# Kernel tuning notes

Hardware: AMD Instinct MI355X
Metric: run time of the kernel (lower is better)

Reference implementation:

```python
import jax, jax.numpy as jnp
import numpy as np

NUM_ENTITY = 500000
NUM_RELATION = 6000
NUM_WORD = 200000
D = 100          # entity_dim == word_dim
L = 3            # num_layer
B, E, F, Q = 16, 2000, 8000, 20
PAGERANK_LAMBDA = 0.8
FACT_SCALE = 3.0
VERY_NEG = -1e11
VERY_SMALL = 1e-10


def setup_inputs() -> dict:
    key = jax.random.key(0)
    ks = jax.random.split(key, 24)
    s = 0.05
    return {
        'local_entity': jax.random.randint(ks[0], (B, E), 0, NUM_ENTITY),
        'kb_fact_rel': jax.random.randint(ks[1], (B, F), 0, NUM_RELATION),
        'kb_head': jax.random.randint(ks[2], (B, F), 0, E),
        'kb_tail': jax.random.randint(ks[3], (B, F), 0, E),
        'query_text': jax.random.randint(ks[4], (B, Q), 0, NUM_WORD),
        'q2e_adj_mat': jax.random.uniform(ks[5], (B, E, 1)),
        'entity_table': jax.random.normal(ks[6], (NUM_ENTITY + 1, D)) * s,
        'rel_table': jax.random.normal(ks[7], (NUM_RELATION + 1, D)) * s,
        'word_table': jax.random.normal(ks[8], (NUM_WORD + 1, D)) * s,
        'rel_lin_w': jax.random.normal(ks[9], (D, D)) * s,
        'rel_lin_b': jnp.zeros((D,)),
        'lstm_wih': jax.random.normal(ks[10], (4 * D, D)) * s,
        'lstm_whh': jax.random.normal(ks[11], (4 * D, D)) * s,
        'lstm_bih': jnp.zeros((4 * D,)),
        'lstm_bhh': jnp.zeros((4 * D,)),
        'q2e_w': jax.random.normal(ks[12], (L, D, D)) * s,
        'q2e_b': jnp.zeros((L, D)),
        'e2q_w': jax.random.normal(ks[13], (L, D, 3 * D)) * s,
        'e2q_b': jnp.zeros((L, D)),
        'e2e_w': jax.random.normal(ks[14], (L, D, 3 * D)) * s,
        'e2e_b': jnp.zeros((L, D)),
        'head_w': jax.random.normal(ks[15], (L, D, D)) * s,
        'head_b': jnp.zeros((L, D)),
        'tail_w': jax.random.normal(ks[16], (L, D, D)) * s,
        'tail_b': jnp.zeros((L, D)),
        'self_w': jax.random.normal(ks[17], (L, D, D)) * s,
        'self_b': jnp.zeros((L, D)),
        'score_w': jax.random.normal(ks[18], (1, D)) * s,
        'score_b': jnp.zeros((1,)),
    }


def _lstm(x, wih, whh, bih, bhh):
    # x: (B, Q, D); torch LSTM gate order i,f,g,o
    b = x.shape[0]
    h0 = jnp.zeros((b, D), x.dtype)

    def step(carry, xt):
        h, c = carry
        g = xt @ wih.T + h @ whh.T + bih + bhh
        i, f, gg, o = jnp.split(g, 4, axis=-1)
        c = jax.nn.sigmoid(f) * c + jax.nn.sigmoid(i) * jnp.tanh(gg)
        h = jax.nn.sigmoid(o) * jnp.tanh(c)
        return (h, c), h

    (h, _), hs = jax.lax.scan(step, (h0, h0), x.transpose(1, 0, 2))
    return hs.transpose(1, 0, 2), h


def _gather(x, idx):
    # sparse_bmm(entity2fact, x): out[b,f] = x[b, head[b,f]]
    return jnp.take_along_axis(x, idx[:, :, None], axis=1)


def _scatter(x, idx, num):
    # sparse_bmm(fact2entity, x): segment-sum facts onto tail entities
    b, f, d = x.shape
    flat = (idx + jnp.arange(b)[:, None] * num).reshape(-1)
    return jax.ops.segment_sum(x.reshape(b * f, d), flat, num_segments=b * num).reshape(b, num, d)


def reference(local_entity, kb_fact_rel, kb_head, kb_tail, query_text, q2e_adj_mat,
              entity_table, rel_table, word_table, rel_lin_w, rel_lin_b,
              lstm_wih, lstm_whh, lstm_bih, lstm_bhh,
              q2e_w, q2e_b, e2q_w, e2q_b, e2e_w, e2e_b,
              head_w, head_b, tail_w, tail_b, self_w, self_b, score_w, score_b):
    div = float(np.sqrt(D))
    q_mask = (query_text != NUM_WORD).astype(jnp.float32)
    e_mask = (local_entity != NUM_ENTITY).astype(jnp.float32)

    # query LSTM encoding
    q_emb = word_table[query_text]                                   # (B,Q,D)
    q_hidden, q_last = _lstm(q_emb, lstm_wih, lstm_whh, lstm_bih, lstm_bhh)
    query_node_emb = q_last[:, None, :]                              # (B,1,D)

    # fact embeddings from relations
    fact_emb = rel_table[kb_fact_rel] @ rel_lin_w.T + rel_lin_b      # (B,F,D)

    # fact-to-query attention weights (softmax over query words)
    sim = jnp.einsum('bqd,bfd->bqf', q_hidden, fact_emb) / div
    sim = jax.nn.softmax(sim + (1.0 - q_mask)[:, :, None] * VERY_NEG, axis=1)
    att = jnp.einsum('bqf,bqd->bfd', sim, q_hidden)                  # (B,F,D)
    Wf = jnp.sum(att * fact_emb, axis=2) / div                       # (B,F)
    W_tilde = jnp.exp(Wf - Wf.max(axis=1, keepdims=True))
    e2f_softmax = jnp.clip(_scatter(W_tilde[:, :, None], kb_head, E)[:, :, 0], VERY_SMALL, None)

    local_entity_emb = entity_table[local_entity]                    # (B,E,D)
    pagerank_f = q2e_adj_mat[:, :, 0]                                # (B,E)

    for i in range(L):
        q2e_emb = jnp.broadcast_to(query_node_emb @ q2e_w[i].T + q2e_b[i], (B, E, D))
        # entity -> fact (gather heads)
        e2f = jax.nn.relu(fact_emb @ self_w[i].T + self_b[i] +
                          _gather(local_entity_emb @ head_w[i].T + head_b[i], kb_head))
        e2f = e2f * (W_tilde[:, :, None] * _gather((pagerank_f / e2f_softmax)[:, :, None], kb_head))
        # fact -> entity (scatter to tails)
        f2e = jax.nn.relu(local_entity_emb @ self_w[i].T + self_b[i] +
                          FACT_SCALE * _scatter(e2f @ tail_w[i].T + tail_b[i], kb_tail, E))
        # pagerank propagation
        pr = _scatter(_gather(pagerank_f[:, :, None], kb_head), kb_tail, E)[:, :, 0]
        pagerank_f = PAGERANK_LAMBDA * pr + (1.0 - PAGERANK_LAMBDA) * pagerank_f
        # k=3 concat -> e2q / e2e updates
        nxt = jnp.concatenate([local_entity_emb, q2e_emb, f2e], axis=2)   # (B,E,3D)
        query_node_emb = jnp.einsum('be,bed->bd', pagerank_f, nxt @ e2q_w[i].T + e2q_b[i])[:, None, :]
        local_entity_emb = jax.nn.relu(nxt @ e2e_w[i].T + e2e_b[i])

    score = (local_entity_emb @ score_w.T + score_b)[:, :, 0]
    return score + (1.0 - e_mask) * VERY_NEG
```

## Files before the change

### kernel.cpp

```cpp
#include <hip/hip_runtime.h>
#include <math.h>

namespace {

typedef unsigned short u16;
typedef short bf16x8 __attribute__((ext_vector_type(8)));
typedef float f32x4 __attribute__((ext_vector_type(4)));

constexpr int B = 16, E = 2000, F = 8000, Q = 20, D = 100, NLAYER = 3;
constexpr int NUM_ENTITY_C = 500000;
constexpr int NREL1 = 6001;
constexpr int SK = 128;
constexpr int WFSZ = 28 * 64 * 8;
constexpr float PAGERANK_LAMBDA = 0.8f;
constexpr float FACT_SCALE = 3.0f;
constexpr float VERY_NEG = -100000000000.0f;
constexpr float VERY_SMALL = 1e-10f;

__device__ __forceinline__ float sigf(float x) { return 1.0f / (1.0f + __expf(-x)); }

__device__ __forceinline__ short f2bf(float f) {
    union { float f; unsigned int u; } c; c.f = f;
    unsigned int u = c.u + 0x7FFF + ((c.u >> 16) & 1);
    return (short)(u >> 16);
}
__device__ __forceinline__ float bf2f(u16 s) {
    union { unsigned int u; float f; } c; c.u = ((unsigned int)s) << 16;
    return c.f;
}

__global__ void wprep_kernel(const float* __restrict__ rel_lin_w,
                             const float* __restrict__ self_w, const float* __restrict__ head_w,
                             const float* __restrict__ tail_w, const float* __restrict__ e2e_w,
                             u16* __restrict__ WF)
{
    int m = blockIdx.y;
    int ns = blockIdx.x;
    int n = ns >> 2, s = ns & 3;
    int lane = threadIdx.x;
    const float* W; int ldW = D, kofs = 0; float scale = 1.f;
    if (m == 0) { W = rel_lin_w; }
    else {
        int L = (m - 1) / 5, t = (m - 1) % 5;
        if (t == 0)      { W = self_w + (size_t)L * D * D; }
        else if (t == 1) { W = head_w + (size_t)L * D * D; }
        else if (t == 2) { W = tail_w + (size_t)L * D * D; scale = FACT_SCALE; }
        else if (t == 3) { W = e2e_w + (size_t)L * D * 3 * D; ldW = 3 * D; }
        else             { W = e2e_w + (size_t)L * D * 3 * D; ldW = 3 * D; kofs = 2 * D; }
    }
    int col = n * 16 + (lane & 15);
    int kb = s * 32 + (lane >> 4) * 8;
    bf16x8 f;
#pragma unroll
    for (int j = 0; j < 8; ++j) {
        int k = kb + j;
        float v = (col < D && k < D) ? scale * W[(size_t)col * ldW + kofs + k] : 0.f;
        f[j] = f2bf(v);
    }
    *reinterpret_cast<bf16x8*>(WF + ((size_t)m * 28 + ns) * 64 * 8 + lane * 8) = f;
}

template<int A1S, int A2S, int EPI, bool OUTBF>
__global__ __launch_bounds__(256, 2) void mm2(
    const void* __restrict__ A1p, const int* __restrict__ idx1, int lda1,
    const void* __restrict__ A2p, const int* __restrict__ idx2,
    const u16* __restrict__ WF1, const u16* __restrict__ WF2,
    const float* __restrict__ b1, const float* __restrict__ b2,
    const float* __restrict__ vq,
    const float* __restrict__ wtv, const float* __restrict__ prv,
    const float* __restrict__ e2fsmv,
    const int* __restrict__ row_start, const int* __restrict__ factlist,
    const float* __restrict__ prOld, const int* __restrict__ headAbs,
    float* __restrict__ prNew,
    void* __restrict__ outp, int nrows)
{
    const int lane = threadIdx.x & 63;
    const int lrow = lane & 15, lkg = lane >> 4;
    const int wv = blockIdx.x * (blockDim.x >> 6) + (threadIdx.x >> 6);
    const int nwv = gridDim.x * (blockDim.x >> 6);
    const int nch = (nrows + 15) >> 4;

    bf16x8 w1[7][4];
#pragma unroll
    for (int n = 0; n < 7; ++n)
#pragma unroll
        for (int s = 0; s < 4; ++s)
            w1[n][s] = *reinterpret_cast<const bf16x8*>(WF1 + ((size_t)(n * 4 + s) * 64 + lane) * 8);

    for (int chunk = wv; chunk < nch; chunk += nwv) {
        const int row = chunk * 16 + lrow;
        const int ar = row < nrows ? row : nrows - 1;

        bf16x8 af1[4];
        if (A1S == 0) {
            const u16* src = (const u16*)A1p + (size_t)ar * SK;
#pragma unroll
            for (int s = 0; s < 4; ++s)
                af1[s] = *reinterpret_cast<const bf16x8*>(src + s * 32 + lkg * 8);
        } else if (A1S == 1) {
            const u16* src = (const u16*)A1p + (size_t)idx1[ar] * SK;
#pragma unroll
            for (int s = 0; s < 4; ++s)
                af1[s] = *reinterpret_cast<const bf16x8*>(src + s * 32 + lkg * 8);
        } else {
            const float* arow = (const float*)A1p + (size_t)ar * lda1;
#pragma unroll
            for (int s = 0; s < 4; ++s) {
                const int k0 = s * 32 + lkg * 8;
                float tv[8];
                if (k0 + 8 <= D) {
                    float4 v0 = *reinterpret_cast<const float4*>(arow + k0);
                    float4 v1 = *reinterpret_cast<const float4*>(arow + k0 + 4);
                    tv[0]=v0.x; tv[1]=v0.y; tv[2]=v0.z; tv[3]=v0.w;
                    tv[4]=v1.x; tv[5]=v1.y; tv[6]=v1.z; tv[7]=v1.w;
                } else {
#pragma unroll
                    for (int j = 0; j < 8; ++j) tv[j] = (k0 + j < D) ? arow[k0 + j] : 0.f;
                }
                bf16x8 f;
#pragma unroll
                for (int j = 0; j < 8; ++j) f[j] = f2bf(tv[j]);
                af1[s] = f;
            }
        }

        bf16x8 af2[4];
        if (A2S == 1) {
            const u16* src = (const u16*)A2p + (size_t)idx2[ar] * SK;
#pragma unroll
            for (int s = 0; s < 4; ++s)
                af2[s] = *reinterpret_cast<const bf16x8*>(src + s * 32 + lkg * 8);
        } else if (A2S == 3) {
            const u16* src = (const u16*)A2p + (size_t)ar * SK;
#pragma unroll
            for (int s = 0; s < 4; ++s)
                af2[s] = *reinterpret_cast<const bf16x8*>(src + s * 32 + lkg * 8);
        } else if (A2S == 2) {
            float a2f[4][8];
#pragma unroll
            for (int s = 0; s < 4; ++s)
#pragma unroll
                for (int j = 0; j < 8; ++j) a2f[s][j] = 0.f;
            const int s0 = row_start[ar], s1 = row_start[ar + 1];
            for (int i = s0; i < s1; ++i) {
                const u16* fr = (const u16*)A2p + (size_t)factlist[i] * SK + lkg * 8;
#pragma unroll
                for (int s = 0; s < 4; ++s) {
                    bf16x8 v = *reinterpret_cast<const bf16x8*>(fr + s * 32);
#pragma unroll
                    for (int j = 0; j < 8; ++j) a2f[s][j] += bf2f((u16)v[j]);
                }
            }
#pragma unroll
            for (int s = 0; s < 4; ++s) {
                bf16x8 f;
#pragma unroll
                for (int j = 0; j < 8; ++j) f[j] = f2bf(a2f[s][j]);
                af2[s] = f;
            }
            if (lkg == 0 && row < nrows) {
                float a = 0.f;
                for (int i = s0; i < s1; ++i) a += prOld[headAbs[factlist[i]]];
                prNew[row] = PAGERANK_LAMBDA * a + (1.0f - PAGERANK_LAMBDA) * prOld[row];
            }
        }

        f32x4 acc[7];
#pragma unroll
        for (int n = 0; n < 7; ++n) acc[n] = (f32x4){0.f, 0.f, 0.f, 0.f};
#pragma unroll
        for (int s = 0; s < 4; ++s) {
#pragma unroll
            for (int n = 0; n < 7; ++n)
                acc[n] = __builtin_amdgcn_mfma_f32_16x16x32_bf16(af1[s], w1[n][s], acc[n], 0, 0, 0);
            if (A2S != 0) {
#pragma unroll
                for (int n = 0; n < 7; ++n) {
                    bf16x8 w2 = *reinterpret_cast<const bf16x8*>(
                        WF2 + ((size_t)(n * 4 + s) * 64 + lane) * 8);
                    acc[n] = __builtin_amdgcn_mfma_f32_16x16x32_bf16(af2[s], w2, acc[n], 0, 0, 0);
                }
            }
        }

        const int rb = chunk * 16 + lkg * 4;
#pragma unroll
        for (int r = 0; r < 4; ++r) {
            const int orow = rb + r;
            if (orow >= nrows) continue;
            float rsv = 1.f, cntf = 0.f; int vb = 0;
            if (EPI == 1) {
                int h = idx2[orow];
                rsv = wtv[orow] * prv[h] / fmaxf(e2fsmv[h], VERY_SMALL);
            }
            if (EPI == 2) cntf = (float)(row_start[orow + 1] - row_start[orow]);
            if (EPI == 3) vb = orow / E;
#pragma unroll
            for (int n = 0; n < 7; ++n) {
                const int col = n * 16 + lrow;
                if (col >= D) continue;
                float v = acc[n][r];
                if (b1) v += b1[col];
                if (EPI == 1) v += b2[col];
                if (EPI == 2) v += FACT_SCALE * cntf * b2[col];
                if (EPI == 3) v += vq[vb * D + col];
                if (EPI != 0) v = fmaxf(v, 0.f);
                if (EPI == 1) v *= rsv;
                if (OUTBF) ((u16*)outp)[(size_t)orow * SK + col] = (u16)f2bf(v);
                else       ((float*)outp)[(size_t)orow * D + col] = v;
            }
        }
    }
}

__global__ __launch_bounds__(512) void gatesx_kernel(
    const int* __restrict__ qtext, const float* __restrict__ wtab,
    const float* __restrict__ wih, const float* __restrict__ bih,
    const float* __restrict__ bhh, float* __restrict__ gx)
{
    int row = blockIdx.x;
    int t = threadIdx.x;
    __shared__ __align__(16) float xs[D];
    if (t < D) xs[t] = wtab[(size_t)qtext[row] * D + t];
    __syncthreads();
    if (t < 4 * D) {
        const float4* w4 = reinterpret_cast<const float4*>(wih + (size_t)t * D);
        const float4* x4 = reinterpret_cast<const float4*>(xs);
        float a0 = 0.f, a1 = 0.f, a2 = 0.f, a3 = 0.f;
#pragma unroll
        for (int k = 0; k < 25; ++k) {
            float4 wv = w4[k]; float4 xv = x4[k];
            a0 = fmaf(wv.x, xv.x, a0); a1 = fmaf(wv.y, xv.y, a1);
            a2 = fmaf(wv.z, xv.z, a2); a3 = fmaf(wv.w, xv.w, a3);
        }
        gx[(size_t)row * (4 * D) + t] = a0 + a1 + a2 + a3 + bih[t] + bhh[t];
    }
}

__global__ __launch_bounds__(512) void lstmrec_kernel(
    const float* __restrict__ gx, const float* __restrict__ whh,
    float* __restrict__ q_hidden, float* __restrict__ qne)
{
    int b = blockIdx.x, t = threadIdx.x;
    __shared__ __align__(16) float h[D];
    __shared__ float cst[D];
    __shared__ float g[4 * D];
    float4 w[25];
    if (t < 4 * D) {
        const float4* wr = reinterpret_cast<const float4*>(whh + (size_t)t * D);
#pragma unroll
        for (int k = 0; k < 25; ++k) w[k] = wr[k];
    }
    if (t < D) { h[t] = 0.f; cst[t] = 0.f; }
    __syncthreads();
    for (int step = 0; step < Q; ++step) {
        if (t < 4 * D) {
            const float4* h4 = reinterpret_cast<const float4*>(h);
            float a0 = 0.f, a1 = 0.f, a2 = 0.f, a3 = 0.f;
#pragma unroll
            for (int k = 0; k < 25; ++k) {
                float4 hv = h4[k];
                a0 = fmaf(w[k].x, hv.x, a0); a1 = fmaf(w[k].y, hv.y, a1);
                a2 = fmaf(w[k].z, hv.z, a2); a3 = fmaf(w[k].w, hv.w, a3);
            }
            g[t] = a0 + a1 + a2 + a3 + gx[((size_t)b * Q + step) * (4 * D) + t];
        }
        __syncthreads();
        if (t < D) {
            float gi = g[t], gf = g[t + D], gg = g[t + 2 * D], go = g[t + 3 * D];
            float cn = sigf(gf) * cst[t] + sigf(gi) * tanhf(gg);
            float hn = sigf(go) * tanhf(cn);
            cst[t] = cn; h[t] = hn;
            q_hidden[((size_t)b * Q + step) * D + t] = hn;
            if (step == Q - 1) qne[b * D + t] = hn;
        }
        __syncthreads();
    }
}

__global__ __launch_bounds__(256) void wf_kernel(const float* __restrict__ qh,
                                                 const u16* __restrict__ REL,
                                                 const int* __restrict__ frel,
                                                 float* __restrict__ Wf)
{
    const int b = blockIdx.y;
    const int f0 = blockIdx.x * 128;
    __shared__ float qs[Q * D];
    __shared__ float fs[128 * 106];
    const int tid = threadIdx.x;
    for (int i = tid; i < Q * D; i += 256) qs[i] = qh[(size_t)b * Q * D + i];
    for (int i = tid; i < 128 * 16; i += 256) {
        int r = i >> 4, c = i & 15;
        if (c < 13 && f0 + r < F) {
            const u16* src = REL + (size_t)frel[b * F + f0 + r] * SK + c * 8;
            bf16x8 raw = *reinterpret_cast<const bf16x8*>(src);
#pragma unroll
            for (int j = 0; j < 8; ++j) fs[r * 106 + c * 8 + j] = bf2f((u16)raw[j]);
        }
    }
    __syncthreads();
    const int f = tid >> 1, half = tid & 1;
    const float* frow = &fs[f * 106 + half * 50];
    float s[Q];
#pragma unroll
    for (int q = 0; q < Q; ++q) {
        const float* qrow = &qs[q * D + half * 50];
        float accv = 0.f;
#pragma unroll 5
        for (int k = 0; k < 50; ++k) accv = fmaf(qrow[k], frow[k], accv);
        accv += __shfl_xor(accv, 1);
        s[q] = accv * 0.1f;
    }
    float mx = s[0];
#pragma unroll
    for (int q = 1; q < Q; ++q) mx = fmaxf(mx, s[q]);
    float sum = 0.f, wf = 0.f;
#pragma unroll
    for (int q = 0; q < Q; ++q) {
        float p = __expf(s[q] - mx);
        sum += p; wf = fmaf(p, s[q], wf);
    }
    wf /= sum;
    if (half == 0 && f0 + f < F) Wf[(size_t)b * F + f0 + f] = wf;
}

__global__ void idxabs_kernel(const int* __restrict__ kb_head, const int* __restrict__ kb_tail,
                              int* __restrict__ headAbs, int* __restrict__ tailAbs,
                              int* __restrict__ counts)
{
    int r = blockIdx.x * 256 + threadIdx.x;
    if (r < B * F) {
        int b = r / F;
        headAbs[r] = b * E + kb_head[r];
        int t = b * E + kb_tail[r];
        tailAbs[r] = t;
        atomicAdd(&counts[t], 1);
    }
}

__global__ __launch_bounds__(1024) void scan_kernel(const int* __restrict__ counts,
                                                    int* __restrict__ row_start,
                                                    int* __restrict__ cursor)
{
    __shared__ int part[1024];
    int t = threadIdx.x;
    int base = t * 32;
    int local[32];
    int s = 0;
#pragma unroll
    for (int i = 0; i < 32; ++i) {
        int idx = base + i;
        int v = (idx < B * E) ? counts[idx] : 0;
        local[i] = s; s += v;
    }
    part[t] = s;
    __syncthreads();
    for (int off = 1; off < 1024; off <<= 1) {
        int v = (t >= off) ? part[t - off] : 0;
        __syncthreads();
        if (t >= off) part[t] += v;
        __syncthreads();
    }
    int prev = (t > 0) ? part[t - 1] : 0;
#pragma unroll
    for (int i = 0; i < 32; ++i) {
        int idx = base + i;
        if (idx < B * E) { int rs = prev + local[i]; row_start[idx] = rs; cursor[idx] = rs; }
    }
    if (t == 1023) row_start[B * E] = part[1023];
}

__global__ void fill_kernel(const int* __restrict__ tailAbs, int* __restrict__ cursor,
                            int* __restrict__ factlist)
{
    int r = blockIdx.x * 256 + threadIdx.x;
    if (r < B * F) {
        int p = atomicAdd(&cursor[tailAbs[r]], 1);
        factlist[p] = r;
    }
}

__global__ void rowmax_kernel(const float* __restrict__ Wf, float* __restrict__ Wmax)
{
    int b = blockIdx.x, tid = threadIdx.x;
    float m = -3.4e38f;
    for (int i = tid; i < F; i += 256) m = fmaxf(m, Wf[(size_t)b * F + i]);
#pragma unroll
    for (int o = 32; o > 0; o >>= 1) m = fmaxf(m, __shfl_down(m, o));
    __shared__ float sm[4];
    if ((tid & 63) == 0) sm[tid >> 6] = m;
    __syncthreads();
    if (tid == 0) Wmax[b] = fmaxf(fmaxf(sm[0], sm[1]), fmaxf(sm[2], sm[3]));
}

__global__ void wtilde_kernel(float* __restrict__ wt, const float* __restrict__ Wmax,
                              const int* __restrict__ headAbs, float* __restrict__ e2fsm)
{
    int r = blockIdx.x * 256 + threadIdx.x;
    if (r < B * F) {
        int b = r / F;
        float v = __expf(wt[r] - Wmax[b]);
        wt[r] = v;
        atomicAdd(&e2fsm[headAbs[r]], v);
    }
}

__global__ void entgather_kernel(const int* __restrict__ local_entity,
                                 const float* __restrict__ etab, u16* __restrict__ emb,
                                 const float* __restrict__ q2e_adj, float* __restrict__ pr)
{
    int i = blockIdx.x * 256 + threadIdx.x;
    if (i < B * E) pr[i] = q2e_adj[i];
    if (i < B * E * 25) {
        int row = i / 25, p = i - row * 25;
        float4 v = reinterpret_cast<const float4*>(etab + (size_t)local_entity[row] * D)[p];
        short4 o;
        o.x = f2bf(v.x); o.y = f2bf(v.y); o.z = f2bf(v.z); o.w = f2bf(v.w);
        *reinterpret_cast<short4*>(emb + (size_t)row * SK + p * 4) = o;
    }
}

__global__ void qvec_kernel(const float* __restrict__ qne, const float* __restrict__ q2ew,
                            const float* __restrict__ q2eb, const float* __restrict__ e2ew,
                            float* __restrict__ q2e_vec, float* __restrict__ vq)
{
    int b = blockIdx.x, t = threadIdx.x;
    __shared__ float qv[D];
    __shared__ float qn[D];
    if (t < D) qn[t] = qne[b * D + t];
    __syncthreads();
    if (t < D) {
        const float* wr = q2ew + (size_t)t * D;
        float acc = q2eb[t];
        for (int k = 0; k < D; ++k) acc = fmaf(qn[k], wr[k], acc);
        qv[t] = acc; q2e_vec[b * D + t] = acc;
    }
    __syncthreads();
    if (t < D) {
        const float* wr = e2ew + (size_t)t * 300 + 100;
        float acc = 0.f;
        for (int k = 0; k < D; ++k) acc = fmaf(qv[k], wr[k], acc);
        vq[b * D + t] = acc;
    }
}

__global__ __launch_bounds__(256) void zsum_kernel(const float* __restrict__ pr,
                                                   const u16* __restrict__ emb,
                                                   const u16* __restrict__ f2e,
                                                   float* __restrict__ zpart)
{
    const int b = blockIdx.x, ch = blockIdx.y;
    const int t = threadIdx.x;
    const int g = t >> 4, tg = t & 15;
    const int ebase = ch * (E / 16);
    const int eend = ebase + (E / 16);
    float accA[8], accB[8];
#pragma unroll
    for (int j = 0; j < 8; ++j) { accA[j] = 0.f; accB[j] = 0.f; }
    float accp = 0.f;
    for (int e = ebase + g; e < eend; e += 16) {
        const float p = pr[b * E + e];
        const size_t ro = ((size_t)b * E + e) * SK + tg * 8;
        bf16x8 va = *reinterpret_cast<const bf16x8*>(emb + ro);
        bf16x8 vb = *reinterpret_cast<const bf16x8*>(f2e + ro);
#pragma unroll
        for (int j = 0; j < 8; ++j) {
            accA[j] = fmaf(p, bf2f((u16)va[j]), accA[j]);
            accB[j] = fmaf(p, bf2f((u16)vb[j]), accB[j]);
        }
        if (tg == 0) accp += p;
    }
    __shared__ float smA[16][132];
    __shared__ float smB[16][132];
    __shared__ float smp[16];
#pragma unroll
    for (int j = 0; j < 8; ++j) {
        smA[g][tg * 8 + j] = accA[j];
        smB[g][tg * 8 + j] = accB[j];
    }
    if (tg == 0) smp[g] = accp;
    __syncthreads();
    float* zp = zpart + (size_t)(b * 16 + ch) * 208;
    if (t < D) {
        float sa = 0.f, sb = 0.f;
#pragma unroll
        for (int gg = 0; gg < 16; ++gg) { sa += smA[gg][t]; sb += smB[gg][t]; }
        zp[t] = sa;
        zp[D + t] = sb;
    }
    if (t == 255) {
        float sp = 0.f;
#pragma unroll
        for (int gg = 0; gg < 16; ++gg) sp += smp[gg];
        zp[2 * D] = sp;
    }
}

__global__ void qne_kernel(const float* __restrict__ zpart, const float* __restrict__ q2ev,
                           const float* __restrict__ W, const float* __restrict__ bias,
                           float* __restrict__ qne)
{
    int b = blockIdx.x, t = threadIdx.x;
    __shared__ float zb[201];
    for (int i = t; i < 201; i += 128) {
        float s = 0.f;
        for (int ch = 0; ch < 16; ++ch) s += zpart[(size_t)(b * 16 + ch) * 208 + i];
        zb[i] = s;
    }
    __syncthreads();
    if (t >= D) return;
    float ps = zb[2 * D];
    const float* wr = W + (size_t)t * 3 * D;
    float acc = ps * bias[t];
    for (int k = 0; k < D; ++k) {
        acc = fmaf(zb[k], wr[k], acc);
        acc = fmaf(ps * q2ev[b * D + k], wr[D + k], acc);
        acc = fmaf(zb[D + k], wr[2 * D + k], acc);
    }
    qne[b * D + t] = acc;
}

__global__ __launch_bounds__(256) void score_kernel(const u16* __restrict__ emb,
                                                    const float* __restrict__ sw,
                                                    const float* __restrict__ sb,
                                                    const int* __restrict__ le,
                                                    float* __restrict__ outp)
{
    __shared__ float rows[64 * 106];
    __shared__ float sws[D];
    int r0 = blockIdx.x * 64, tid = threadIdx.x;
    for (int i = tid; i < 64 * 16; i += 256) {
        int r = i >> 4, c = i & 15;
        if (c < 13) {
            bf16x8 raw = *reinterpret_cast<const bf16x8*>(emb + (size_t)(r0 + r) * SK + c * 8);
#pragma unroll
            for (int j = 0; j < 8; ++j) rows[r * 106 + c * 8 + j] = bf2f((u16)raw[j]);
        }
    }
    if (tid < D) sws[tid] = sw[tid];
    __syncthreads();
    if (tid < 64) {
        float acc = sb[0];
        const float* rr = &rows[tid * 106];
        for (int k = 0; k < D; ++k) acc = fmaf(rr[k], sws[k], acc);
        int r = r0 + tid;
        outp[r] = acc + ((le[r] != NUM_ENTITY_C) ? 0.0f : VERY_NEG);
    }
}

int mmgrid(int nrows) {
    int ch = (nrows + 15) / 16;
    int blocks = (ch + 3) / 4;
    return blocks < 512 ? blocks : 512;
}

}

extern "C" void kernel_launch(void* const* d_in, const int* in_sizes, int n_in,
                              void* d_out, int out_size, void* d_ws, size_t ws_size,
                              hipStream_t stream)
{
    (void)in_sizes; (void)n_in; (void)out_size;
    const int*   local_entity = (const int*)d_in[0];
    const int*   kb_fact_rel  = (const int*)d_in[1];
    const int*   kb_head      = (const int*)d_in[2];
    const int*   kb_tail      = (const int*)d_in[3];
    const int*   query_text   = (const int*)d_in[4];
    const float* q2e_adj      = (const float*)d_in[5];
    const float* entity_table = (const float*)d_in[6];
    const float* rel_table    = (const float*)d_in[7];
    const float* word_table   = (const float*)d_in[8];
    const float* rel_lin_w    = (const float*)d_in[9];
    const float* rel_lin_b    = (const float*)d_in[10];
    const float* lstm_wih     = (const float*)d_in[11];
    const float* lstm_whh     = (const float*)d_in[12];
    const float* lstm_bih     = (const float*)d_in[13];
    const float* lstm_bhh     = (const float*)d_in[14];
    const float* q2e_w        = (const float*)d_in[15];
    const float* q2e_b        = (const float*)d_in[16];
    const float* e2q_w        = (const float*)d_in[17];
    const float* e2q_b        = (const float*)d_in[18];
    const float* e2e_w        = (const float*)d_in[19];
    const float* e2e_b        = (const float*)d_in[20];
    const float* head_w       = (const float*)d_in[21];
    const float* head_b       = (const float*)d_in[22];
    const float* tail_w       = (const float*)d_in[23];
    const float* tail_b       = (const float*)d_in[24];
    const float* self_w       = (const float*)d_in[25];
    const float* self_b       = (const float*)d_in[26];
    const float* score_w      = (const float*)d_in[27];
    const float* score_b      = (const float*)d_in[28];
    float* out = (float*)d_out;

    float* ws = (float*)d_ws;
    size_t o = 0;
    auto alloc = [&](size_t n) { float* p = ws + o; o += (n + 3) & ~(size_t)3; return p; };
    float* q_hidden = alloc((size_t)B * Q * D);
    float* qne      = alloc(B * D);
    float* gx       = alloc((size_t)B * Q * 4 * D);
    float* wt       = alloc((size_t)B * F);
    float* wmax     = alloc(16);
    float* e2fsm    = alloc(B * E);
    float* pr0      = alloc(B * E);
    float* pr1      = alloc(B * E);
    float* q2e_vec  = alloc(B * D);
    float* vq       = alloc(B * D);
    float* zpart    = alloc((size_t)B * 16 * 208);
    u16* WF   = (u16*)alloc((size_t)16 * WFSZ / 2);
    u16* REL  = (u16*)alloc((size_t)NREL1 * SK / 2 + 64);
    u16* emb0 = (u16*)alloc((size_t)B * E * SK / 2);
    u16* emb1 = (u16*)alloc((size_t)B * E * SK / 2);
    u16* e2f  = (u16*)alloc((size_t)B * F * SK / 2);
    u16* f2e  = (u16*)alloc((size_t)B * E * SK / 2);
    int* headAbs  = (int*)alloc((size_t)B * F);
    int* tailAbs  = (int*)alloc((size_t)B * F);
    int* counts   = (int*)alloc(B * E);
    int* row_start= (int*)alloc(B * E + 1);
    int* cursor   = (int*)alloc(B * E);
    int* factlist = (int*)alloc((size_t)B * F);
    if (ws_size < o * sizeof(float)) return;

    auto WFm = [&](int m) { return WF + (size_t)m * WFSZ; };

    wprep_kernel<<<dim3(28, 16), dim3(64), 0, stream>>>(rel_lin_w, self_w, head_w, tail_w,
                                                        e2e_w, WF);
    gatesx_kernel<<<dim3(B * Q), dim3(512), 0, stream>>>(query_text, word_table, lstm_wih,
                                                         lstm_bih, lstm_bhh, gx);
    lstmrec_kernel<<<dim3(B), dim3(512), 0, stream>>>(gx, lstm_whh, q_hidden, qne);
    hipMemsetAsync(counts, 0, (size_t)B * E * sizeof(int), stream);
    idxabs_kernel<<<dim3((B * F + 255) / 256), dim3(256), 0, stream>>>(
        kb_head, kb_tail, headAbs, tailAbs, counts);
    scan_kernel<<<dim3(1), dim3(1024), 0, stream>>>(counts, row_start, cursor);
    fill_kernel<<<dim3((B * F + 255) / 256), dim3(256), 0, stream>>>(tailAbs, cursor, factlist);

    mm2<2, 0, 0, true><<<dim3(mmgrid(NREL1)), dim3(256), 0, stream>>>(
        rel_table, nullptr, D, nullptr, nullptr, WFm(0), nullptr, rel_lin_b, nullptr,
        nullptr, nullptr, nullptr, nullptr, nullptr, nullptr, nullptr, nullptr, nullptr,
        REL, NREL1);

    wf_kernel<<<dim3((F + 127) / 128, B), dim3(256), 0, stream>>>(q_hidden, REL, kb_fact_rel, wt);
    rowmax_kernel<<<dim3(B), dim3(256), 0, stream>>>(wt, wmax);
    hipMemsetAsync(e2fsm, 0, (size_t)B * E * sizeof(float), stream);
    wtilde_kernel<<<dim3((B * F + 255) / 256), dim3(256), 0, stream>>>(wt, wmax, headAbs, e2fsm);
    entgather_kernel<<<dim3((B * E * 25 + 255) / 256), dim3(256), 0, stream>>>(
        local_entity, entity_table, emb0, q2e_adj, pr0);

    u16* embO = emb0; u16* embN = emb1;
    float* prO = pr0; float* prN = pr1;
    for (int i = 0; i < NLAYER; ++i) {
        const float* q2e_wi  = q2e_w + (size_t)i * D * D;
        const float* q2e_bi  = q2e_b + i * D;
        const float* e2q_wi  = e2q_w + (size_t)i * D * 3 * D;
        const float* e2q_bi  = e2q_b + i * D;
        const float* e2e_wi  = e2e_w + (size_t)i * D * 3 * D;
        const float* e2e_bi  = e2e_b + i * D;
        const float* head_bi = head_b + i * D;
        const float* tail_bi = tail_b + i * D;
        const float* self_bi = self_b + i * D;
        const u16* wf_self = WFm(1 + i * 5 + 0);
        const u16* wf_head = WFm(1 + i * 5 + 1);
        const u16* wf_tail = WFm(1 + i * 5 + 2);
        const u16* wf_e2e0 = WFm(1 + i * 5 + 3);
        const u16* wf_e2e2 = WFm(1 + i * 5 + 4);

        qvec_kernel<<<dim3(B), dim3(128), 0, stream>>>(qne, q2e_wi, q2e_bi, e2e_wi,
                                                       q2e_vec, vq);
        mm2<1, 1, 1, true><<<dim3(mmgrid(B * F)), dim3(256), 0, stream>>>(
            REL, kb_fact_rel, 0, embO, headAbs, wf_self, wf_head, self_bi, head_bi,
            nullptr, wt, prO, e2fsm, nullptr, nullptr, nullptr, nullptr, nullptr,
            e2f, B * F);
        mm2<0, 2, 2, true><<<dim3(mmgrid(B * E)), dim3(256), 0, stream>>>(
            embO, nullptr, 0, e2f, nullptr, wf_self, wf_tail, self_bi, tail_bi,
            nullptr, nullptr, nullptr, nullptr, row_start, factlist, prO, headAbs, prN,
            f2e, B * E);
        zsum_kernel<<<dim3(B, 16), dim3(256), 0, stream>>>(prN, embO, f2e, zpart);
        qne_kernel<<<dim3(B), dim3(128), 0, stream>>>(zpart, q2e_vec, e2q_wi, e2q_bi, qne);
        mm2<0, 3, 3, true><<<dim3(mmgrid(B * E)), dim3(256), 0, stream>>>(
            embO, nullptr, 0, f2e, nullptr, wf_e2e0, wf_e2e2, e2e_bi, nullptr,
            vq, nullptr, nullptr, nullptr, nullptr, nullptr, nullptr, nullptr, nullptr,
            embN, B * E);
        { u16* tmp = embO; embO = embN; embN = tmp; }
        { float* tmp = prO; prO = prN; prN = tmp; }
    }
    score_kernel<<<dim3((B * E) / 64), dim3(256), 0, stream>>>(
        embO, score_w, score_b, local_entity, out);
}
```

Measured before the change: 687.3 us.

## Store fact embeddings in tail-sorted order to make scatter reads contiguous

```diff
diff --git a/kernel.cpp b/kernel.cpp
--- a/kernel.cpp
+++ b/kernel.cpp
@@ -68,9 +68,8 @@
     const float* __restrict__ b1, const float* __restrict__ b2,
     const float* __restrict__ vq,
     const float* __restrict__ wtv, const float* __restrict__ prv,
-    const float* __restrict__ e2fsmv,
-    const int* __restrict__ row_start, const int* __restrict__ factlist,
-    const float* __restrict__ prOld, const int* __restrict__ headAbs,
+    const int* __restrict__ row_start,
+    const float* __restrict__ prOld, const int* __restrict__ sheadv,
     float* __restrict__ prNew,
     void* __restrict__ outp, int nrows)
 {
@@ -124,6 +123,9 @@
             }
         }
 
+        int s0 = 0, s1 = 0;
+        if (A2S == 2) { s0 = row_start[ar]; s1 = row_start[ar + 1]; }
+
         bf16x8 af2[4];
         if (A2S == 1) {
             const u16* src = (const u16*)A2p + (size_t)idx2[ar] * SK;
@@ -135,34 +137,6 @@
 #pragma unroll
             for (int s = 0; s < 4; ++s)
                 af2[s] = *reinterpret_cast<const bf16x8*>(src + s * 32 + lkg * 8);
-        } else if (A2S == 2) {
-            float a2f[4][8];
-#pragma unroll
-            for (int s = 0; s < 4; ++s)
-#pragma unroll
-                for (int j = 0; j < 8; ++j) a2f[s][j] = 0.f;
-            const int s0 = row_start[ar], s1 = row_start[ar + 1];
-            for (int i = s0; i < s1; ++i) {
-                const u16* fr = (const u16*)A2p + (size_t)factlist[i] * SK + lkg * 8;
-#pragma unroll
-                for (int s = 0; s < 4; ++s) {
-                    bf16x8 v = *reinterpret_cast<const bf16x8*>(fr + s * 32);
-#pragma unroll
-                    for (int j = 0; j < 8; ++j) a2f[s][j] += bf2f((u16)v[j]);
-                }
-            }
-#pragma unroll
-            for (int s = 0; s < 4; ++s) {
-                bf16x8 f;
-#pragma unroll
-                for (int j = 0; j < 8; ++j) f[j] = f2bf(a2f[s][j]);
-                af2[s] = f;
-            }
-            if (lkg == 0 && row < nrows) {
-                float a = 0.f;
-                for (int i = s0; i < s1; ++i) a += prOld[headAbs[factlist[i]]];
-                prNew[row] = PAGERANK_LAMBDA * a + (1.0f - PAGERANK_LAMBDA) * prOld[row];
-            }
         }
 
         f32x4 acc[7];
@@ -173,14 +147,38 @@
 #pragma unroll
             for (int n = 0; n < 7; ++n)
                 acc[n] = __builtin_amdgcn_mfma_f32_16x16x32_bf16(af1[s], w1[n][s], acc[n], 0, 0, 0);
-            if (A2S != 0) {
+            if (A2S == 1 || A2S == 3) {
 #pragma unroll
                 for (int n = 0; n < 7; ++n) {
                     bf16x8 w2 = *reinterpret_cast<const bf16x8*>(
                         WF2 + ((size_t)(n * 4 + s) * 64 + lane) * 8);
                     acc[n] = __builtin_amdgcn_mfma_f32_16x16x32_bf16(af2[s], w2, acc[n], 0, 0, 0);
                 }
+            } else if (A2S == 2) {
+                float a2f[8];
+#pragma unroll
+                for (int j = 0; j < 8; ++j) a2f[j] = 0.f;
+                for (int i = s0; i < s1; ++i) {
+                    bf16x8 v = *reinterpret_cast<const bf16x8*>(
+                        (const u16*)A2p + (size_t)i * SK + s * 32 + lkg * 8);
+#pragma unroll
+                    for (int j = 0; j < 8; ++j) a2f[j] += bf2f((u16)v[j]);
+                }
+                bf16x8 fsum;
+#pragma unroll
+                for (int j = 0; j < 8; ++j) fsum[j] = f2bf(a2f[j]);
+#pragma unroll
+                for (int n = 0; n < 7; ++n) {
+                    bf16x8 w2 = *reinterpret_cast<const bf16x8*>(
+                        WF2 + ((size_t)(n * 4 + s) * 64 + lane) * 8);
+                    acc[n] = __builtin_amdgcn_mfma_f32_16x16x32_bf16(fsum, w2, acc[n], 0, 0, 0);
+                }
             }
+        }
+        if (A2S == 2 && lkg == 0 && row < nrows) {
+            float a = 0.f;
+            for (int i = s0; i < s1; ++i) a += prOld[sheadv[i]];
+            prNew[row] = PAGERANK_LAMBDA * a + (1.0f - PAGERANK_LAMBDA) * prOld[row];
         }
 
         const int rb = chunk * 16 + lkg * 4;
@@ -189,10 +187,7 @@
             const int orow = rb + r;
             if (orow >= nrows) continue;
             float rsv = 1.f, cntf = 0.f; int vb = 0;
-            if (EPI == 1) {
-                int h = idx2[orow];
-                rsv = wtv[orow] * prv[h] / fmaxf(e2fsmv[h], VERY_SMALL);
-            }
+            if (EPI == 1) rsv = wtv[orow] * prv[idx2[orow]];
             if (EPI == 2) cntf = (float)(row_start[orow + 1] - row_start[orow]);
             if (EPI == 3) vb = orow / E;
 #pragma unroll
@@ -300,14 +295,19 @@
     }
     __syncthreads();
     const int f = tid >> 1, half = tid & 1;
-    const float* frow = &fs[f * 106 + half * 50];
+    float fr[50];
+    {
+        const float* frow = &fs[f * 106 + half * 50];
+#pragma unroll
+        for (int k = 0; k < 50; ++k) fr[k] = frow[k];
+    }
     float s[Q];
 #pragma unroll
     for (int q = 0; q < Q; ++q) {
         const float* qrow = &qs[q * D + half * 50];
         float accv = 0.f;
 #pragma unroll 5
-        for (int k = 0; k < 50; ++k) accv = fmaf(qrow[k], frow[k], accv);
+        for (int k = 0; k < 50; ++k) accv = fmaf(qrow[k], fr[k], accv);
         accv += __shfl_xor(accv, 1);
         s[q] = accv * 0.1f;
     }
@@ -377,6 +377,22 @@
     if (r < B * F) {
         int p = atomicAdd(&cursor[tailAbs[r]], 1);
         factlist[p] = r;
+    }
+}
+
+__global__ void sprep_kernel(const int* __restrict__ factlist, const int* __restrict__ frel,
+                             const int* __restrict__ headAbs, const float* __restrict__ wt,
+                             const float* __restrict__ e2fsm,
+                             int* __restrict__ srel, int* __restrict__ shead,
+                             float* __restrict__ srsv)
+{
+    int i = blockIdx.x * 256 + threadIdx.x;
+    if (i < B * F) {
+        int fl = factlist[i];
+        int h = headAbs[fl];
+        srel[i] = frel[fl];
+        shead[i] = h;
+        srsv[i] = wt[fl] / fmaxf(e2fsm[h], VERY_SMALL);
     }
 }
 
@@ -551,7 +567,7 @@
 int mmgrid(int nrows) {
     int ch = (nrows + 15) / 16;
     int blocks = (ch + 3) / 4;
-    return blocks < 512 ? blocks : 512;
+    return blocks < 2048 ? blocks : 2048;
 }
 
 }
@@ -601,23 +617,26 @@
     float* wt       = alloc((size_t)B * F);
     float* wmax     = alloc(16);
     float* e2fsm    = alloc(B * E);
+    int*   counts   = (int*)alloc(B * E);
     float* pr0      = alloc(B * E);
     float* pr1      = alloc(B * E);
     float* q2e_vec  = alloc(B * D);
     float* vq       = alloc(B * D);
     float* zpart    = alloc((size_t)B * 16 * 208);
+    float* srsv     = alloc((size_t)B * F);
     u16* WF   = (u16*)alloc((size_t)16 * WFSZ / 2);
     u16* REL  = (u16*)alloc((size_t)NREL1 * SK / 2 + 64);
     u16* emb0 = (u16*)alloc((size_t)B * E * SK / 2);
     u16* emb1 = (u16*)alloc((size_t)B * E * SK / 2);
-    u16* e2f  = (u16*)alloc((size_t)B * F * SK / 2);
+    u16* e2fS = (u16*)alloc((size_t)B * F * SK / 2);
     u16* f2e  = (u16*)alloc((size_t)B * E * SK / 2);
     int* headAbs  = (int*)alloc((size_t)B * F);
     int* tailAbs  = (int*)alloc((size_t)B * F);
-    int* counts   = (int*)alloc(B * E);
     int* row_start= (int*)alloc(B * E + 1);
     int* cursor   = (int*)alloc(B * E);
     int* factlist = (int*)alloc((size_t)B * F);
+    int* srel     = (int*)alloc((size_t)B * F);
+    int* shead    = (int*)alloc((size_t)B * F);
     if (ws_size < o * sizeof(float)) return;
 
     auto WFm = [&](int m) { return WF + (size_t)m * WFSZ; };
@@ -627,7 +646,7 @@
     gatesx_kernel<<<dim3(B * Q), dim3(512), 0, stream>>>(query_text, word_table, lstm_wih,
                                                          lstm_bih, lstm_bhh, gx);
     lstmrec_kernel<<<dim3(B), dim3(512), 0, stream>>>(gx, lstm_whh, q_hidden, qne);
-    hipMemsetAsync(counts, 0, (size_t)B * E * sizeof(int), stream);
+    hipMemsetAsync(e2fsm, 0, (size_t)2 * B * E * sizeof(float), stream);
     idxabs_kernel<<<dim3((B * F + 255) / 256), dim3(256), 0, stream>>>(
         kb_head, kb_tail, headAbs, tailAbs, counts);
     scan_kernel<<<dim3(1), dim3(1024), 0, stream>>>(counts, row_start, cursor);
@@ -635,13 +654,14 @@
 
     mm2<2, 0, 0, true><<<dim3(mmgrid(NREL1)), dim3(256), 0, stream>>>(
         rel_table, nullptr, D, nullptr, nullptr, WFm(0), nullptr, rel_lin_b, nullptr,
-        nullptr, nullptr, nullptr, nullptr, nullptr, nullptr, nullptr, nullptr, nullptr,
+        nullptr, nullptr, nullptr, nullptr, nullptr, nullptr, nullptr,
         REL, NREL1);
 
     wf_kernel<<<dim3((F + 127) / 128, B), dim3(256), 0, stream>>>(q_hidden, REL, kb_fact_rel, wt);
     rowmax_kernel<<<dim3(B), dim3(256), 0, stream>>>(wt, wmax);
-    hipMemsetAsync(e2fsm, 0, (size_t)B * E * sizeof(float), stream);
     wtilde_kernel<<<dim3((B * F + 255) / 256), dim3(256), 0, stream>>>(wt, wmax, headAbs, e2fsm);
+    sprep_kernel<<<dim3((B * F + 255) / 256), dim3(256), 0, stream>>>(
+        factlist, kb_fact_rel, headAbs, wt, e2fsm, srel, shead, srsv);
     entgather_kernel<<<dim3((B * E * 25 + 255) / 256), dim3(256), 0, stream>>>(
         local_entity, entity_table, emb0, q2e_adj, pr0);
 
@@ -666,18 +686,18 @@
         qvec_kernel<<<dim3(B), dim3(128), 0, stream>>>(qne, q2e_wi, q2e_bi, e2e_wi,
                                                        q2e_vec, vq);
         mm2<1, 1, 1, true><<<dim3(mmgrid(B * F)), dim3(256), 0, stream>>>(
-            REL, kb_fact_rel, 0, embO, headAbs, wf_self, wf_head, self_bi, head_bi,
-            nullptr, wt, prO, e2fsm, nullptr, nullptr, nullptr, nullptr, nullptr,
-            e2f, B * F);
+            REL, srel, 0, embO, shead, wf_self, wf_head, self_bi, head_bi,
+            nullptr, srsv, prO, nullptr, nullptr, nullptr, nullptr,
+            e2fS, B * F);
         mm2<0, 2, 2, true><<<dim3(mmgrid(B * E)), dim3(256), 0, stream>>>(
-            embO, nullptr, 0, e2f, nullptr, wf_self, wf_tail, self_bi, tail_bi,
-            nullptr, nullptr, nullptr, nullptr, row_start, factlist, prO, headAbs, prN,
+            embO, nullptr, 0, e2fS, nullptr, wf_self, wf_tail, self_bi, tail_bi,
+            nullptr, nullptr, nullptr, row_start, prO, shead, prN,
             f2e, B * E);
         zsum_kernel<<<dim3(B, 16), dim3(256), 0, stream>>>(prN, embO, f2e, zpart);
         qne_kernel<<<dim3(B), dim3(128), 0, stream>>>(zpart, q2e_vec, e2q_wi, e2q_bi, qne);
         mm2<0, 3, 3, true><<<dim3(mmgrid(B * E)), dim3(256), 0, stream>>>(
             embO, nullptr, 0, f2e, nullptr, wf_e2e0, wf_e2e2, e2e_bi, nullptr,
-            vq, nullptr, nullptr, nullptr, nullptr, nullptr, nullptr, nullptr, nullptr,
+            vq, nullptr, nullptr, nullptr, nullptr, nullptr, nullptr,
             embN, B * E);
         { u16* tmp = embO; embO = embN; embN = tmp; }
         { float* tmp = prO; prO = prN; prN = tmp; }
```

Result: slower. 793.3 us (+15.4%).
